# Optimization experiments

Hardware: AMD Instinct MI355X
Metric: run time of the kernel (lower is better)

Reference implementation:

```python
import jax, jax.numpy as jnp
import numpy as np

H, W = 14, 14
MIN_RATIO, MAX_RATIO = 0.25, 1.0
GLOBAL_RATIO = 0.5


def setup_inputs() -> dict:
    key = jax.random.key(0)
    motion = jax.random.uniform(key, (512, 1, 224, 224), dtype=jnp.float32)
    return {"motion_magnitude": motion, "num_tokens": 6272}


def reference(motion_magnitude, num_tokens):
    B, C, Hin, Win = motion_magnitude.shape
    # adaptive_avg_pool2d to (14,14): input dims are exact multiples -> block mean
    fh, fw = Hin // H, Win // W
    motion_resized = motion_magnitude.reshape(B, C, H, fh, W, fw).mean(axis=(3, 5))  # (B,1,H,W)
    m_min = motion_resized.min()
    m_max = motion_resized.max()
    motion_normalized = (motion_resized - m_min) / (m_max - m_min + 1e-6)
    importance_scores = motion_normalized[:, 0]  # (B,H,W)
    compression_ratio = MIN_RATIO + (MAX_RATIO - MIN_RATIO) * importance_scores
    current_avg = compression_ratio.mean()
    scale = GLOBAL_RATIO / (current_avg + 1e-6)
    scaled = jnp.clip(compression_ratio * scale, MIN_RATIO, MAX_RATIO)
    compression_ratio = jnp.where(current_avg > 0, scaled, compression_ratio)

    # --- vectorized get_merge_indices (replaces double Python loop) ---
    ratio_flat = compression_ratio.reshape(B, H * W)
    tpp = num_tokens // (H * W)  # tokens per patch
    k = jnp.clip(jnp.round(ratio_flat * tpp).astype(jnp.int32), 1, tpp)  # (B,HW)
    # keep first k tokens inside each patch's contiguous block of tpp tokens
    within = jnp.arange(tpp, dtype=jnp.int32)  # (tpp,)
    mask = (within[None, None, :] < k[:, :, None]).astype(jnp.float32)  # (B,HW,tpp)
    merge_mask = mask.reshape(B, H * W * tpp)
    if H * W * tpp < num_tokens:  # pad remainder with zeros (kept at 0 in original)
        merge_mask = jnp.pad(merge_mask, ((0, 0), (0, num_tokens - H * W * tpp)))
    return compression_ratio, importance_scores, merge_mask
```

## Files before the change

### kernel.cpp

```cpp
#include <hip/hip_runtime.h>
#include <math.h>

#define HW2   196
#define IMG   224
#define IMG2  (224*224)
#define SPB   4

typedef float f32x4 __attribute__((ext_vector_type(4)));

__global__ __launch_bounds__(256) void k_patch_mean(const float* __restrict__ in,
                                                    float* __restrict__ resized,
                                                    float* __restrict__ pmin,
                                                    float* __restrict__ pmax,
                                                    float* __restrict__ psum,
                                                    int nstrips) {
    const int t    = threadIdx.x;
    const int wid  = t >> 6;
    const int lane = t & 63;
    const int s    = blockIdx.x * SPB + wid;

    f32x4 acc = (f32x4)(0.f);
    if (s < nstrips && lane < 56) {
        const f32x4* strip = (const f32x4*)(in + (size_t)s * (16 * IMG)) + lane;
        #pragma unroll
        for (int r = 0; r < 16; ++r) {
            f32x4 v = __builtin_nontemporal_load(&strip[r * 56]);
            acc += v;
        }
    }
    float h = (acc.x + acc.y) + (acc.z + acc.w);
    h += __shfl_xor(h, 1, 64);
    h += __shfl_xor(h, 2, 64);
    float g = __shfl(h, lane * 4, 64);

    __shared__ float means[SPB * 14];
    if (s < nstrips && lane < 14) {
        float mean = g * (1.0f / 256.0f);
        resized[s * 14 + lane] = mean;
        means[wid * 14 + lane] = mean;
    }
    __syncthreads();

    if (wid == 0) {
        float mnv = INFINITY, mxv = -INFINITY, sv = 0.0f;
        if (lane < SPB * 14) {
            int s2 = blockIdx.x * SPB + (lane / 14);
            if (s2 < nstrips) {
                float m = means[lane];
                mnv = m; mxv = m; sv = m;
            }
        }
        #pragma unroll
        for (int off = 32; off; off >>= 1) {
            mnv = fminf(mnv, __shfl_xor(mnv, off, 64));
            mxv = fmaxf(mxv, __shfl_xor(mxv, off, 64));
            sv += __shfl_xor(sv, off, 64);
        }
        if (lane == 0) {
            pmin[blockIdx.x] = mnv;
            pmax[blockIdx.x] = mxv;
            psum[blockIdx.x] = sv;
        }
    }
}

__global__ __launch_bounds__(256) void k_scalars(const float* __restrict__ pmin,
                                                 const float* __restrict__ pmax,
                                                 const float* __restrict__ psum,
                                                 int nblk1, int npair,
                                                 float* __restrict__ sc3) {
    int t = threadIdx.x;
    float  mn = INFINITY, mx = -INFINITY;
    double s  = 0.0;
    for (int i = t; i < nblk1; i += 256) {
        mn = fminf(mn, pmin[i]);
        mx = fmaxf(mx, pmax[i]);
        s += (double)psum[i];
    }
    #pragma unroll
    for (int off = 32; off; off >>= 1) {
        mn = fminf(mn, __shfl_xor(mn, off, 64));
        mx = fmaxf(mx, __shfl_xor(mx, off, 64));
        s += __shfl_xor(s, off, 64);
    }
    __shared__ float  smn[4], smx[4];
    __shared__ double ssm[4];
    int wid = t >> 6, lane = t & 63;
    if (lane == 0) { smn[wid] = mn; smx[wid] = mx; ssm[wid] = s; }
    __syncthreads();
    if (t == 0) {
        mn = fminf(fminf(smn[0], smn[1]), fminf(smn[2], smn[3]));
        mx = fmaxf(fmaxf(smx[0], smx[1]), fmaxf(smx[2], smx[3]));
        s  = ssm[0] + ssm[1] + ssm[2] + ssm[3];
        float denom = __fadd_rn(__fsub_rn(mx, mn), 1e-6f);
        double mean     = s / (double)npair;
        double avg_norm = (mean - (double)mn) / (double)denom;
        double cur_avg  = 0.25 + 0.75 * avg_norm;
        sc3[0] = mn;
        sc3[1] = denom;
        sc3[2] = (float)(0.5 / (cur_avg + 1e-6));
    }
}

__global__ __launch_bounds__(256) void k_output(const float* __restrict__ resized,
                                                const float* __restrict__ sc3,
                                                float* __restrict__ out,
                                                int npair, int tpp, int num_tokens) {
    int t = threadIdx.x;
    const float fmn = sc3[0], fden = sc3[1], fscale = sc3[2];

    int base = blockIdx.x * 256;
    int g = base + t;
    __shared__ int      kk[256];
    __shared__ unsigned kbase[256];
    int k = 0;
    unsigned kb = 0;
    if (g < npair) {
        float r = resized[g];
        float norm   = __fdiv_rn(__fsub_rn(r, fmn), fden);
        float ratio0 = __fadd_rn(0.25f, __fmul_rn(0.75f, norm));
        float sc     = __fmul_rn(ratio0, fscale);
        float ratio  = fminf(fmaxf(sc, 0.25f), 1.0f);
        k = (int)rintf(__fmul_rn(ratio, (float)tpp));
        k = min(max(k, 1), tpp);
        out[g]         = ratio;
        out[npair + g] = norm;
        unsigned b = (unsigned)g / HW2;
        unsigned p = (unsigned)g - b * HW2;
        kb = b * (unsigned)num_tokens + p * (unsigned)tpp;
    }
    kk[t]    = k;
    kbase[t] = kb;
    __syncthreads();

    float* mask = out + 2 * (size_t)npair;
    int nprs = min(256, npair - base);
    if ((tpp & 3) == 0) {
        int tq = tpp >> 2;
        int total4 = nprs * tq;
        for (int i = t; i < total4; i += 256) {
            int pr = (unsigned)i / (unsigned)tq;
            int wi = (i - pr * tq) * 4;
            int kv = kk[pr];
            float4 m;
            m.x = (wi     < kv) ? 1.0f : 0.0f;
            m.y = (wi + 1 < kv) ? 1.0f : 0.0f;
            m.z = (wi + 2 < kv) ? 1.0f : 0.0f;
            m.w = (wi + 3 < kv) ? 1.0f : 0.0f;
            *(float4*)(mask + (size_t)kbase[pr] + wi) = m;
        }
    } else {
        int total = nprs * tpp;
        for (int i = t; i < total; i += 256) {
            int pr = (unsigned)i / (unsigned)tpp;
            int wi = i - pr * tpp;
            mask[(size_t)kbase[pr] + wi] = (wi < kk[pr]) ? 1.0f : 0.0f;
        }
    }
}

__global__ void k_pad(float* __restrict__ mask, int B, int num_tokens, int used) {
    int per = num_tokens - used;
    int idx = blockIdx.x * 256 + threadIdx.x;
    int tot = B * per;
    if (idx < tot) {
        int b = idx / per;
        int j = idx - b * per;
        mask[(size_t)b * num_tokens + used + j] = 0.0f;
    }
}

extern "C" void kernel_launch(void* const* d_in, const int* in_sizes, int n_in,
                              void* d_out, int out_size, void* d_ws, size_t ws_size,
                              hipStream_t stream) {
    const float* motion = (const float*)d_in[0];
    int nelem = in_sizes[0];
    int B     = nelem / IMG2;
    int npair = B * HW2;
    int num_tokens = (out_size - 2 * npair) / B;
    int tpp   = num_tokens / HW2;

    int nstrips = npair / 14;
    int nb1 = (nstrips + SPB - 1) / SPB;

    float* resized = (float*)d_ws;
    float* psum = resized + npair;
    float* pmin = psum + nb1;
    float* pmax = pmin + nb1;
    float* sc3  = pmax + nb1;

    hipLaunchKernelGGL(k_patch_mean, dim3(nb1), dim3(256), 0, stream,
                       motion, resized, pmin, pmax, psum, nstrips);

    hipLaunchKernelGGL(k_scalars, dim3(1), dim3(256), 0, stream,
                       pmin, pmax, psum, nb1, npair, sc3);

    int nb2 = (npair + 255) / 256;
    hipLaunchKernelGGL(k_output, dim3(nb2), dim3(256), 0, stream,
                       resized, sc3, (float*)d_out, npair, tpp, num_tokens);

    int used = HW2 * tpp;
    if (used < num_tokens) {
        int tot = B * (num_tokens - used);
        hipLaunchKernelGGL(k_pad, dim3((tot + 255) / 256), dim3(256), 0, stream,
                           (float*)d_out + 2 * (size_t)npair, B, num_tokens, used);
    }
}
```

Before: 28.22 us.

## Stage input via global_load_lds and fold scalar reduction into output kernel

The patch-mean kernel now pulls two 16-row strips per block into LDS with direct global-to-LDS loads, and all four waves reduce half-strips from LDS instead of each wave streaming one strip from global memory. The single-block scalar kernel is removed: every output block redundantly reduces the per-block min/max/sum partials itself, which drops one launch and its serialization. The cost is that each of the 392 output blocks rereads the partial arrays, and the partial arrays are now twice as large. The bounds checks on strip count are removed, so the code assumes the strip count divides evenly by two.

```diff
diff --git a/kernel.cpp b/kernel.cpp
--- a/kernel.cpp
+++ b/kernel.cpp
@@ -4,7 +4,8 @@
 #define HW2   196
 #define IMG   224
 #define IMG2  (224*224)
-#define SPB   4
+#define SPB   2
+#define STAGEF (SPB*16*IMG)
 
 typedef float f32x4 __attribute__((ext_vector_type(4)));
 
@@ -12,43 +13,46 @@
                                                     float* __restrict__ resized,
                                                     float* __restrict__ pmin,
                                                     float* __restrict__ pmax,
-                                                    float* __restrict__ psum,
-                                                    int nstrips) {
+                                                    float* __restrict__ psum) {
+    __shared__ float smem[STAGEF];
+    __shared__ float halfsums[4][14];
+
     const int t    = threadIdx.x;
     const int wid  = t >> 6;
     const int lane = t & 63;
-    const int s    = blockIdx.x * SPB + wid;
-
+
+    const float* gsrc = in + (size_t)blockIdx.x * STAGEF;
+    #pragma unroll
+    for (int i = 0; i < 7; ++i) {
+        int chunk = i * 4 + wid;
+        const float* gp = gsrc + chunk * 256 + lane * 4;
+        float* lp = smem + chunk * 256;
+        __builtin_amdgcn_global_load_lds(gp, lp, 16, 0, 0);
+    }
+    __syncthreads();
+
+    const int sl = wid >> 1;
+    const int r0 = (wid & 1) * 8;
     f32x4 acc = (f32x4)(0.f);
-    if (s < nstrips && lane < 56) {
-        const f32x4* strip = (const f32x4*)(in + (size_t)s * (16 * IMG)) + lane;
+    if (lane < 56) {
+        const f32x4* base = (const f32x4*)(smem + sl * (16 * IMG)) + lane;
         #pragma unroll
-        for (int r = 0; r < 16; ++r) {
-            f32x4 v = __builtin_nontemporal_load(&strip[r * 56]);
-            acc += v;
-        }
+        for (int r = 0; r < 8; ++r) acc += base[(r0 + r) * 56];
     }
     float h = (acc.x + acc.y) + (acc.z + acc.w);
     h += __shfl_xor(h, 1, 64);
     h += __shfl_xor(h, 2, 64);
-    float g = __shfl(h, lane * 4, 64);
-
-    __shared__ float means[SPB * 14];
-    if (s < nstrips && lane < 14) {
-        float mean = g * (1.0f / 256.0f);
-        resized[s * 14 + lane] = mean;
-        means[wid * 14 + lane] = mean;
-    }
+    if (lane < 56 && (lane & 3) == 0) halfsums[wid][lane >> 2] = h;
     __syncthreads();
 
     if (wid == 0) {
         float mnv = INFINITY, mxv = -INFINITY, sv = 0.0f;
         if (lane < SPB * 14) {
-            int s2 = blockIdx.x * SPB + (lane / 14);
-            if (s2 < nstrips) {
-                float m = means[lane];
-                mnv = m; mxv = m; sv = m;
-            }
+            int s2 = lane / 14, p = lane - s2 * 14;
+            float mean = (halfsums[2 * s2][p] + halfsums[2 * s2 + 1][p])
+                         * (1.0f / 256.0f);
+            resized[blockIdx.x * (SPB * 14) + lane] = mean;
+            mnv = mean; mxv = mean; sv = mean;
         }
         #pragma unroll
         for (int off = 32; off; off >>= 1) {
@@ -64,11 +68,13 @@
     }
 }
 
-__global__ __launch_bounds__(256) void k_scalars(const float* __restrict__ pmin,
-                                                 const float* __restrict__ pmax,
-                                                 const float* __restrict__ psum,
-                                                 int nblk1, int npair,
-                                                 float* __restrict__ sc3) {
+__global__ __launch_bounds__(256) void k_output(const float* __restrict__ resized,
+                                                const float* __restrict__ pmin,
+                                                const float* __restrict__ pmax,
+                                                const float* __restrict__ psum,
+                                                int nblk1,
+                                                float* __restrict__ out,
+                                                int npair, int tpp, int num_tokens) {
     int t = threadIdx.x;
     float  mn = INFINITY, mx = -INFINITY;
     double s  = 0.0;
@@ -85,6 +91,7 @@
     }
     __shared__ float  smn[4], smx[4];
     __shared__ double ssm[4];
+    __shared__ float  sc3[3];
     int wid = t >> 6, lane = t & 63;
     if (lane == 0) { smn[wid] = mn; smx[wid] = mx; ssm[wid] = s; }
     __syncthreads();
@@ -100,13 +107,7 @@
         sc3[1] = denom;
         sc3[2] = (float)(0.5 / (cur_avg + 1e-6));
     }
-}
-
-__global__ __launch_bounds__(256) void k_output(const float* __restrict__ resized,
-                                                const float* __restrict__ sc3,
-                                                float* __restrict__ out,
-                                                int npair, int tpp, int num_tokens) {
-    int t = threadIdx.x;
+    __syncthreads();
     const float fmn = sc3[0], fden = sc3[1], fscale = sc3[2];
 
     int base = blockIdx.x * 256;
@@ -181,23 +182,20 @@
     int tpp   = num_tokens / HW2;
 
     int nstrips = npair / 14;
-    int nb1 = (nstrips + SPB - 1) / SPB;
+    int nb1 = nstrips / SPB;
 
     float* resized = (float*)d_ws;
     float* psum = resized + npair;
     float* pmin = psum + nb1;
     float* pmax = pmin + nb1;
-    float* sc3  = pmax + nb1;
 
     hipLaunchKernelGGL(k_patch_mean, dim3(nb1), dim3(256), 0, stream,
-                       motion, resized, pmin, pmax, psum, nstrips);
-
-    hipLaunchKernelGGL(k_scalars, dim3(1), dim3(256), 0, stream,
-                       pmin, pmax, psum, nb1, npair, sc3);
+                       motion, resized, pmin, pmax, psum);
 
     int nb2 = (npair + 255) / 256;
     hipLaunchKernelGGL(k_output, dim3(nb2), dim3(256), 0, stream,
-                       resized, sc3, (float*)d_out, npair, tpp, num_tokens);
+                       resized, pmin, pmax, psum, nb1,
+                       (float*)d_out, npair, tpp, num_tokens);
 
     int used = HW2 * tpp;
     if (used < num_tokens) {
```

After: 30.75 us. 1.09x slower.
